# Performance work log

Measured on AMD Instinct MI355X. Metric: run time of the kernel, lower is better.

## Reference

```python
import jax, jax.numpy as jnp
import numpy as np

KERNEL_LEN = 512
INPUT_LEN = 65536


def setup_inputs() -> dict:
    key = jax.random.key(0)
    k1, k2 = jax.random.split(key)
    x = jax.random.normal(k1, (INPUT_LEN,), dtype=jnp.float32)
    kernel = jax.random.normal(k2, (KERNEL_LEN,), dtype=jnp.float32)
    return {"input": x, "kernel": kernel}


def _dtw_row(prev, d_row):
    # prev: accumulated_cost of previous row, shape [K]
    # ac[j] = min(prev[j-1], prev[j], ac[j-1]) + d[j]
    # Let c[j] = min(prev[j-1], prev[j]) + d[j]  (prev[-1] treated as +inf,
    # which reproduces ac[i,0] = prev[0] + d[0]).
    # Then ac[j] = min(c[j], ac[j-1] + d[j])
    #            = S[j] + cummin_k<=j (c[k] - S[k]),  S = inclusive cumsum of d.
    inf = jnp.full((1,), jnp.inf, dtype=d_row.dtype)
    prev_shift = jnp.concatenate([inf, prev[:-1]])
    c = jnp.minimum(prev_shift, prev) + d_row
    S = jnp.cumsum(d_row)
    ac = S + jax.lax.cummin(c - S)
    return ac, ac[-1]


def reference(input, kernel):
    # pairwise squared distances: [input_len, kernel_len]
    d = (kernel[None, :] - input[:, None]) ** 2
    # row 0: cumulative sum along kernel axis
    prev0 = jnp.cumsum(d[0])
    # rows 1..N-1 via scan with wavefront-free min-plus row update
    _, lasts = jax.lax.scan(_dtw_row, prev0, d[1:])
    # return accumulated_cost[:, kernel_len - 1]
    return jnp.concatenate([prev0[-1:], lasts])
```

## Files before the change

kernel.cpp:

```cpp
#include <hip/hip_runtime.h>


#define K_LEN 512
#define N_LEN 65536
#define PAD_L 512
#define PAD_R 1024
#define XPAD_TOTAL (PAD_L + N_LEN + PAD_R)
#define BIGX 1e20f
#define NCHUNK 1032
#define RING 256

__global__ void dtw_pad_kernel(const float* __restrict__ x, float* __restrict__ xpad) {
    int i = blockIdx.x * blockDim.x + threadIdx.x;
    if (i < XPAD_TOTAL) {
        int j = i - PAD_L;
        xpad[i] = (j >= 0 && j < N_LEN) ? x[j] : BIGX;
    }
}

template <bool LAST>
__device__ __forceinline__ void dtw_chunk(int c, const float* __restrict__ xl,
                                          const float* __restrict__ ldsIn,
                                          float* __restrict__ ldsOut,
                                          float k0, float k1,
                                          float& A0, float& A1, float& E0, float& E1,
                                          float& xp, int lane, float* __restrict__ out) {
    const int t0 = c * 64;
    const int rb = (c & 3) * 64;

    float xv[64];
#pragma unroll
    for (int r = 0; r < 64; ++r) xv[r] = xl[t0 + r];

    float binv[64];
    binv[0] = ldsIn[(rb + RING - 1) & (RING - 1)];
#pragma unroll
    for (int r = 1; r < 64; ++r) binv[r] = ldsIn[rb + r - 1];

    float keep[64];

#pragma unroll
    for (int r = 0; r < 64; ++r) {
        const float xf = xv[r];
        const float esh0 = __int_as_float(__builtin_amdgcn_update_dpp(
            __float_as_int(binv[r]), __float_as_int(E1), 0x138 , 0xF, 0xF, false));
        const float esh1 = E0;
        float d0 = k0 - xf; d0 *= d0;
        float d1 = k1 - xp; d1 *= d1;
        const float na0 = fminf(A0, esh0) + d0;
        const float na1 = fminf(A1, esh1) + d1;
        const float ne0 = fminf(na0, A0);
        const float ne1 = fminf(na1, A1);
        keep[r] = LAST ? na1 : ne1;
        A0 = na0; A1 = na1; E0 = ne0; E1 = ne1; xp = xf;
    }

    if (lane == 63) {
#pragma unroll
        for (int r = 0; r < 64; ++r) ldsOut[rb + r] = keep[r];
    }

    if (LAST) {
        const float ov = ldsOut[rb + lane];
        const int oi = t0 + lane - (K_LEN - 1);
        if (oi >= 0 && oi < N_LEN) out[oi] = ov;
    }
}

__global__ __launch_bounds__(256, 1) void dtw_main(const float* __restrict__ xpad,
                                                   const float* __restrict__ kern,
                                                   float* __restrict__ out) {
    __shared__ float lds[5 * RING];
    const float INFV = __builtin_inff();
    const int tid  = threadIdx.x;
    const int w    = __builtin_amdgcn_readfirstlane(tid) >> 6;
    const int lane = tid & 63;

    for (int i = tid; i < 5 * RING; i += 256)
        lds[i] = (i == 4 * RING + RING - 1) ? 0.0f : INFV;
    __syncthreads();

    const int j0 = w * 128 + 2 * lane;
    const float k0 = kern[j0];
    const float k1 = kern[j0 + 1];

    const float* xl = xpad + (PAD_L - j0);
    float xp = xl[-1];

    float* ldsOut      = lds + w * RING;
    const float* ldsIn = (w == 0) ? (lds + 4 * RING) : (lds + (w - 1) * RING);

    float A0 = INFV, A1 = INFV, E0 = INFV, E1 = INFV;

    for (int S = 0; S < NCHUNK + 3; ++S) {
        const int c = S - w;
        if (c >= 0 && c < NCHUNK) {
            if (w == 3)
                dtw_chunk<true>(c, xl, ldsIn, ldsOut, k0, k1, A0, A1, E0, E1, xp, lane, out);
            else
                dtw_chunk<false>(c, xl, ldsIn, ldsOut, k0, k1, A0, A1, E0, E1, xp, lane, out);
        }
        if (S == 0 && tid == 0) lds[4 * RING + RING - 1] = INFV;
        __syncthreads();
    }
}

extern "C" void kernel_launch(void* const* d_in, const int* in_sizes, int n_in,
                              void* d_out, int out_size, void* d_ws, size_t ws_size,
                              hipStream_t stream) {
    const float* x = (const float*)d_in[0];
    const float* k = (const float*)d_in[1];
    float* xpad = (float*)d_ws;
    float* out  = (float*)d_out;
    dtw_pad_kernel<<<(XPAD_TOTAL + 255) / 256, 256, 0, stream>>>(x, xpad);
    dtw_main<<<1, 256, 0, stream>>>(xpad, k, out);
}
```

Baseline: 2.129 ms.

## Stream x and boundary values through DPP lane shifts instead of per-lane loads

Each lane no longer loads 64 x values and 64 LDS boundary values into register arrays per chunk. Instead one coalesced value per lane is loaded, and the values are shifted across lanes with DPP row-shift each step, so x propagates diagonally through the wavefront. The last-lane outputs are likewise accumulated via DPP shifts into a per-lane register and written with a single coalesced store. This cuts global/LDS traffic and register pressure, at the cost of extra DPP ops on the serial dependency chain.

```diff
diff --git a/kernel.cpp b/kernel.cpp
--- a/kernel.cpp
+++ b/kernel.cpp
@@ -10,6 +10,10 @@
 #define NCHUNK 1032
 #define RING 256
 
+#define DPPF(old, src, ctrl)                                                     \
+    __int_as_float(__builtin_amdgcn_update_dpp(                                  \
+        __float_as_int(old), __float_as_int(src), (ctrl), 0xF, 0xF, false))
+
 __global__ void dtw_pad_kernel(const float* __restrict__ x, float* __restrict__ xpad) {
     int i = blockIdx.x * blockDim.x + threadIdx.x;
     if (i < XPAD_TOTAL) {
@@ -19,51 +23,46 @@
 }
 
 template <bool LAST>
-__device__ __forceinline__ void dtw_chunk(int c, const float* __restrict__ xl,
+__device__ __forceinline__ void dtw_chunk(int c, float& Xa, const float* __restrict__ xlw,
                                           const float* __restrict__ ldsIn,
                                           float* __restrict__ ldsOut,
                                           float k0, float k1,
                                           float& A0, float& A1, float& E0, float& E1,
-                                          float& xp, int lane, float* __restrict__ out) {
+                                          float& xA, float& xB, int lane,
+                                          float* __restrict__ out) {
     const int t0 = c * 64;
     const int rb = (c & 3) * 64;
 
-    float xv[64];
-#pragma unroll
-    for (int r = 0; r < 64; ++r) xv[r] = xl[t0 + r];
+    const float Xb = xlw[t0 + 64 + lane];
 
-    float binv[64];
-    binv[0] = ldsIn[(rb + RING - 1) & (RING - 1)];
-#pragma unroll
-    for (int r = 1; r < 64; ++r) binv[r] = ldsIn[rb + r - 1];
+    float B = ldsIn[(rb + lane + RING - 1) & (RING - 1)];
 
-    float keep[64];
+    float X = Xa;
+    float C = 0.0f;
 
 #pragma unroll
     for (int r = 0; r < 64; ++r) {
-        const float xf = xv[r];
-        const float esh0 = __int_as_float(__builtin_amdgcn_update_dpp(
-            __float_as_int(binv[r]), __float_as_int(E1), 0x138 , 0xF, 0xF, false));
-        const float esh1 = E0;
-        float d0 = k0 - xf; d0 *= d0;
-        float d1 = k1 - xp; d1 *= d1;
+        const float xnew = DPPF(X, xB, 0x138);
+        const float esh0 = DPPF(B, E1, 0x138);
+        X = DPPF(X, X, 0x130);
+        B = DPPF(B, B, 0x130);
+        float d0 = k0 - xnew; d0 *= d0;
+        float d1 = k1 - xA;   d1 *= d1;
         const float na0 = fminf(A0, esh0) + d0;
-        const float na1 = fminf(A1, esh1) + d1;
+        const float na1 = fminf(A1, E0) + d1;
         const float ne0 = fminf(na0, A0);
         const float ne1 = fminf(na1, A1);
-        keep[r] = LAST ? na1 : ne1;
-        A0 = na0; A1 = na1; E0 = ne0; E1 = ne1; xp = xf;
+        C = DPPF(LAST ? na1 : ne1, C, 0x130);
+        A0 = na0; A1 = na1; E0 = ne0; E1 = ne1;
+        xB = xA; xA = xnew;
     }
 
-    if (lane == 63) {
-#pragma unroll
-        for (int r = 0; r < 64; ++r) ldsOut[rb + r] = keep[r];
-    }
-
-    if (LAST) {
-        const float ov = ldsOut[rb + lane];
+    Xa = Xb;
+    if (!LAST) {
+        ldsOut[rb + lane] = C;
+    } else {
         const int oi = t0 + lane - (K_LEN - 1);
-        if (oi >= 0 && oi < N_LEN) out[oi] = ov;
+        if (oi >= 0 && oi < N_LEN) out[oi] = C;
     }
 }
 
@@ -84,8 +83,11 @@
     const float k0 = kern[j0];
     const float k1 = kern[j0 + 1];
 
-    const float* xl = xpad + (PAD_L - j0);
-    float xp = xl[-1];
+    const float* xl  = xpad + PAD_L - j0;
+    const float* xlw = xpad + PAD_L - w * 128;
+    float xA = xl[-1];
+    float xB = xl[-2];
+    float Xa = xlw[lane];
 
     float* ldsOut      = lds + w * RING;
     const float* ldsIn = (w == 0) ? (lds + 4 * RING) : (lds + (w - 1) * RING);
@@ -96,9 +98,9 @@
         const int c = S - w;
         if (c >= 0 && c < NCHUNK) {
             if (w == 3)
-                dtw_chunk<true>(c, xl, ldsIn, ldsOut, k0, k1, A0, A1, E0, E1, xp, lane, out);
+                dtw_chunk<true>(c, Xa, xlw, ldsIn, ldsOut, k0, k1, A0, A1, E0, E1, xA, xB, lane, out);
             else
-                dtw_chunk<false>(c, xl, ldsIn, ldsOut, k0, k1, A0, A1, E0, E1, xp, lane, out);
+                dtw_chunk<false>(c, Xa, xlw, ldsIn, ldsOut, k0, k1, A0, A1, E0, E1, xA, xB, lane, out);
         }
         if (S == 0 && tid == 0) lds[4 * RING + RING - 1] = INFV;
         __syncthreads();
```

Result: slower. 2.277 ms (+7.0%).

## Double-buffer x prefetch and pass boundary/output values through lanes

Applied to the files above, without the earlier changes.

Loads for the next chunk's x values are issued as float2 vector loads into a second register buffer, so they overlap the current chunk's 64-step recurrence. The 64 per-step LDS reads of the neighbour wave's boundary value become one LDS load per lane, read back with readlane. The lane-63-only store of 64 values is replaced by a DPP shift that collects the results into a register, written with one coalesced store. The squared distance and add are fused into an FMA. This cuts LDS traffic and memory latency on the serial dependency chain, at the cost of more registers and extra readlane/DPP ops in each step.

```diff
diff --git a/kernel.cpp b/kernel.cpp
--- a/kernel.cpp
+++ b/kernel.cpp
@@ -20,6 +20,7 @@
 
 template <bool LAST>
 __device__ __forceinline__ void dtw_chunk(int c, const float* __restrict__ xl,
+                                          float2 (&xc)[32], float2 (&xn)[32],
                                           const float* __restrict__ ldsIn,
                                           float* __restrict__ ldsOut,
                                           float k0, float k1,
@@ -28,42 +29,43 @@
     const int t0 = c * 64;
     const int rb = (c & 3) * 64;
 
-    float xv[64];
+    const float2* xnp = reinterpret_cast<const float2*>(xl + t0 + 64);
 #pragma unroll
-    for (int r = 0; r < 64; ++r) xv[r] = xl[t0 + r];
+    for (int q = 0; q < 32; ++q) xn[q] = xnp[q];
 
-    float binv[64];
-    binv[0] = ldsIn[(rb + RING - 1) & (RING - 1)];
-#pragma unroll
-    for (int r = 1; r < 64; ++r) binv[r] = ldsIn[rb + r - 1];
+    const float B = ldsIn[(rb + lane + RING - 1) & (RING - 1)];
 
-    float keep[64];
+    float C = 0.0f;
 
 #pragma unroll
     for (int r = 0; r < 64; ++r) {
-        const float xf = xv[r];
-        const float esh0 = __int_as_float(__builtin_amdgcn_update_dpp(
-            __float_as_int(binv[r]), __float_as_int(E1), 0x138 , 0xF, 0xF, false));
-        const float esh1 = E0;
-        float d0 = k0 - xf; d0 *= d0;
-        float d1 = k1 - xp; d1 *= d1;
-        const float na0 = fminf(A0, esh0) + d0;
-        const float na1 = fminf(A1, esh1) + d1;
+        const float xf = (r & 1) ? xc[r >> 1].y : xc[r >> 1].x;
+        const int sbi = __builtin_amdgcn_readlane(__float_as_int(B), r);
+        const float eshs = __int_as_float(__builtin_amdgcn_update_dpp(
+            0, __float_as_int(E1), 0x138 , 0xF, 0xF, true));
+        const float esh0 = (lane != 0) ? eshs : __int_as_float(sbi);
+
+        const float t0c = k0 - xf;
+        const float t1c = k1 - xp;
+        const float m0  = fminf(A0, esh0);
+        const float m1  = fminf(A1, E0);
+        const float na0 = __builtin_fmaf(t0c, t0c, m0);
+        const float na1 = __builtin_fmaf(t1c, t1c, m1);
         const float ne0 = fminf(na0, A0);
         const float ne1 = fminf(na1, A1);
-        keep[r] = LAST ? na1 : ne1;
+
+        const float keepv = LAST ? na1 : ne1;
+        C = __int_as_float(__builtin_amdgcn_update_dpp(
+            __float_as_int(keepv), __float_as_int(C), 0x130 , 0xF, 0xF, false));
+
         A0 = na0; A1 = na1; E0 = ne0; E1 = ne1; xp = xf;
     }
 
-    if (lane == 63) {
-#pragma unroll
-        for (int r = 0; r < 64; ++r) ldsOut[rb + r] = keep[r];
-    }
-
-    if (LAST) {
-        const float ov = ldsOut[rb + lane];
+    if (!LAST) {
+        ldsOut[rb + lane] = C;
+    } else {
         const int oi = t0 + lane - (K_LEN - 1);
-        if (oi >= 0 && oi < N_LEN) out[oi] = ov;
+        if (oi >= 0 && oi < N_LEN) out[oi] = C;
     }
 }
 
@@ -84,7 +86,7 @@
     const float k0 = kern[j0];
     const float k1 = kern[j0 + 1];
 
-    const float* xl = xpad + (PAD_L - j0);
+    const float* xl = xpad + PAD_L - j0;
     float xp = xl[-1];
 
     float* ldsOut      = lds + w * RING;
@@ -92,13 +94,23 @@
 
     float A0 = INFV, A1 = INFV, E0 = INFV, E1 = INFV;
 
+    float2 xwA[32], xwB[32];
+    {
+        const float2* x0p = reinterpret_cast<const float2*>(xl);
+#pragma unroll
+        for (int q = 0; q < 32; ++q) xwA[q] = x0p[q];
+    }
+
     for (int S = 0; S < NCHUNK + 3; ++S) {
         const int c = S - w;
         if (c >= 0 && c < NCHUNK) {
-            if (w == 3)
-                dtw_chunk<true>(c, xl, ldsIn, ldsOut, k0, k1, A0, A1, E0, E1, xp, lane, out);
-            else
-                dtw_chunk<false>(c, xl, ldsIn, ldsOut, k0, k1, A0, A1, E0, E1, xp, lane, out);
+            if (c & 1) {
+                if (w == 3) dtw_chunk<true >(c, xl, xwB, xwA, ldsIn, ldsOut, k0, k1, A0, A1, E0, E1, xp, lane, out);
+                else        dtw_chunk<false>(c, xl, xwB, xwA, ldsIn, ldsOut, k0, k1, A0, A1, E0, E1, xp, lane, out);
+            } else {
+                if (w == 3) dtw_chunk<true >(c, xl, xwA, xwB, ldsIn, ldsOut, k0, k1, A0, A1, E0, E1, xp, lane, out);
+                else        dtw_chunk<false>(c, xl, xwA, xwB, ldsIn, ldsOut, k0, k1, A0, A1, E0, E1, xp, lane, out);
+            }
         }
         if (S == 0 && tid == 0) lds[4 * RING + RING - 1] = INFV;
         __syncthreads();
```

Result: slower. 2.253 ms (+5.8%).
